# Optimization experiments

Measured on AMD Instinct MI355X. Metric: run time of the kernel, lower is better.

The kernel has to match this reference:

```python
import jax, jax.numpy as jnp
import numpy as np

B, T, H, L, FUT = 64, 256, 512, 4, 64


def setup_inputs() -> dict:
    key = jax.random.key(0)
    ks = jax.random.split(key, 8)
    s = 1.0 / np.sqrt(H)  # PyTorch LSTMCell/Linear default uniform init bound
    u = lambda k, shape: jax.random.uniform(k, shape, jnp.float32, -s, s)
    return {
        "iput": jax.random.normal(ks[0], (B, T), jnp.float32),
        "W_ih0": u(ks[1], (4 * H, 1)),        # layer 0 input->gates
        "W_ih": u(ks[2], (L - 1, 4 * H, H)),  # layers 1..L-1 input->gates
        "W_hh": u(ks[3], (L, 4 * H, H)),      # hidden->gates, all layers
        "b_ih": u(ks[4], (L, 4 * H)),
        "b_hh": u(ks[5], (L, 4 * H)),
        "W_lin": u(ks[6], (1, H)),            # readout Linear(H, 1)
        "b_lin": u(ks[7], (1,)),
        "future": FUT,
    }


def _cell(x, h, c, Wi, Wh, bi, bh):
    # PyTorch LSTMCell: gates ordered i, f, g, o
    g = x @ Wi.T + h @ Wh.T + bi + bh  # [B, 4H]
    i, f, gg, o = jnp.split(g, 4, axis=-1)
    c2 = jax.nn.sigmoid(f) * c + jax.nn.sigmoid(i) * jnp.tanh(gg)
    h2 = jax.nn.sigmoid(o) * jnp.tanh(c2)
    return h2, c2


def reference(iput, W_ih0, W_ih, W_hh, b_ih, b_hh, W_lin, b_lin, future):
    Lc = W_hh.shape[0]
    Bsz = iput.shape[0]
    Hd = W_hh.shape[-1]

    def layers(x, hs, cs):  # x: [B,1]; hs,cs: [L,B,H]
        for j in range(Lc):
            Wi = W_ih0 if j == 0 else W_ih[j - 1]
            inp = x if j == 0 else hs[j - 1]
            h2, c2 = _cell(inp, hs[j], cs[j], Wi, W_hh[j], b_ih[j], b_hh[j])
            hs = hs.at[j].set(h2)
            cs = cs.at[j].set(c2)
        return hs, cs

    hs0 = jnp.zeros((Lc, Bsz, Hd), iput.dtype)
    cs0 = jnp.zeros_like(hs0)

    def step_in(carry, x_t):  # x_t: [B]
        hs, cs = carry
        hs, cs = layers(x_t[:, None], hs, cs)
        out = hs[-1] @ W_lin.T + b_lin  # [B,1]
        return (hs, cs), out[:, 0]

    (hs, cs), outs = jax.lax.scan(step_in, (hs0, cs0), iput.T)  # outs: [T,B]

    def step_fut(carry, _):
        hs, cs, out = carry
        hs, cs = layers(out, hs, cs)
        out2 = hs[-1] @ W_lin.T + b_lin
        return (hs, cs, out2), out2[:, 0]

    last_out = outs[-1][:, None]  # feed last prediction back
    _, fouts = jax.lax.scan(step_fut, (hs, cs, last_out), None, length=future)

    return jnp.concatenate([outs, fouts], axis=0).T  # [B, T+future]
```

## Files before the change

kernel.cpp:

```cpp
#include <hip/hip_runtime.h>

#define Bsz 64
#define Tn 256
#define Hn 512
#define Ln 4
#define Gn 2048
#define TTn 320
#define NBLK 256
#define NTHR 1024
#define HB (Hn * Bsz)
#define LHB (Ln * HB)
#define NPH_W (Tn + Ln - 1)

typedef float f32x4 __attribute__((ext_vector_type(4)));

#define OFF_WHH  0
#define OFF_WIH  (OFF_WHH + Ln * 8 * Hn)
#define OFF_PART (OFF_WIH + (Ln - 1) * 8 * Hn)
#define OFF_BS   (OFF_PART + 4 * 8 * Bsz)
#define OFF_W0   (OFF_BS + Ln * 8)
#define OFF_WLIN (OFF_W0 + 8)
#define OFF_RP   (OFF_WLIN + Hn)
#define OFF_XS   (OFF_RP + 16 * Bsz)
#define OFF_C    (OFF_XS + Bsz)
#define SMEM_FLOATS (OFF_C + Ln * 2 * Bsz)
#define SMEM_BYTES (SMEM_FLOATS * 4)

#define WS_BCOUNT   0
#define WS_ARRIVE   16
#define WS_MASTER   (16 + 16 * 32)
#define WS_BOOT     (WS_MASTER + 32)
#define WS_BOOTFLAG (WS_BOOT + 32)
#define WS_U32S     (WS_BOOTFLAG + 32)

__device__ float g_h[2 * LHB];
__device__ float g_hist[Tn * HB];
__device__ float g_p[Bsz * NBLK];
__device__ float g_xsg[Bsz];

__device__ __forceinline__ float sigm(float x) { return 1.0f / (1.0f + expf(-x)); }

__device__ __forceinline__ void fma4v(f32x4& a, const f32x4 h, const float w) {
    a.x = fmaf(h.x, w, a.x); a.y = fmaf(h.y, w, a.y);
    a.z = fmaf(h.z, w, a.z); a.w = fmaf(h.w, w, a.w);
}

#define GSTF(ptr, val) \
    asm volatile("global_store_dword %0, %1, off sc0 sc1" \
                 :: "v"(ptr), "v"(val) : "memory")
#define VMWAIT() asm volatile("s_waitcnt vmcnt(0)" ::: "memory")
#define L1INV() asm volatile("buffer_inv" ::: "memory")

__device__ __forceinline__ uint32_t rmw_add(uint32_t* p, uint32_t v) {
    return __hip_atomic_fetch_add(p, v, __ATOMIC_RELAXED, __HIP_MEMORY_SCOPE_AGENT);
}
__device__ __forceinline__ uint32_t ald(const uint32_t* p) {
    return __hip_atomic_load(p, __ATOMIC_RELAXED, __HIP_MEMORY_SCOPE_AGENT);
}
__device__ __forceinline__ uint32_t xcc_id() {
    uint32_t x;
    asm("s_getreg_b32 %0, hwreg(HW_REG_XCC_ID)" : "=s"(x));
    return x & 15u;
}

__device__ __forceinline__ void boot_bar(uint32_t* wsb, int tid) {
    VMWAIT();
    __syncthreads();
    if (tid == 0) {
        __builtin_amdgcn_fence(__ATOMIC_RELEASE, "agent");
        uint32_t old = rmw_add(wsb + WS_BOOT, 1u);
        if (old == NBLK - 1u) rmw_add(wsb + WS_BOOTFLAG, 1u);
        while (ald(wsb + WS_BOOTFLAG) < 1u) __builtin_amdgcn_s_sleep(2);
        __builtin_amdgcn_fence(__ATOMIC_ACQUIRE, "agent");
    }
    __syncthreads();
    asm volatile("" ::: "memory");
}

__device__ __forceinline__ void gbar(uint32_t* wsb, int tid, uint32_t x,
                                     uint32_t cnt_x, uint32_t& e) {
    ++e;
    VMWAIT();
    __syncthreads();
    if (tid == 0) {
        const uint32_t tgt = e * (uint32_t)NBLK;
        uint32_t old = rmw_add(wsb + WS_ARRIVE + x * 32, 1u);
        if (old == e * cnt_x - 1u) {
            __builtin_amdgcn_fence(__ATOMIC_ACQUIRE, "agent");
            VMWAIT();
            rmw_add(wsb + WS_MASTER, cnt_x);
            while (ald(wsb + WS_MASTER) < tgt) {}
        } else {
            while (ald(wsb + WS_MASTER) < tgt) {}
            L1INV();
            VMWAIT();
        }
    }
    __syncthreads();
    asm volatile("" ::: "memory");
}

template <int NITER>
__device__ __forceinline__ void gemm_rows2(const float* __restrict__ wrow,
                                           const float* __restrict__ hbase,
                                           int k0, int rot, int b4,
                                           f32x4& a0, f32x4& a1) {
#pragma unroll 4
    for (int c = 0; c < NITER; ++c) {
        const int cc = (c + rot) & (NITER - 1);
        const int k = k0 + cc * 4;
        const float* hp = hbase + (size_t)k * Bsz + b4;
        const f32x4 h0 = *(const f32x4*)(hp);
        const f32x4 h1 = *(const f32x4*)(hp + Bsz);
        const f32x4 h2 = *(const f32x4*)(hp + 2 * Bsz);
        const f32x4 h3 = *(const f32x4*)(hp + 3 * Bsz);
        const f32x4 w0 = *(const f32x4*)(wrow + k);
        const f32x4 w1 = *(const f32x4*)(wrow + Hn + k);
        fma4v(a0, h0, w0.x); fma4v(a0, h1, w0.y);
        fma4v(a0, h2, w0.z); fma4v(a0, h3, w0.w);
        fma4v(a1, h0, w1.x); fma4v(a1, h1, w1.y);
        fma4v(a1, h2, w1.z); fma4v(a1, h3, w1.w);
    }
}

__device__ __forceinline__ void wave_reduce2(f32x4& a0, f32x4& a1) {
    a0.x += __shfl_xor(a0.x, 16); a0.y += __shfl_xor(a0.y, 16);
    a0.z += __shfl_xor(a0.z, 16); a0.w += __shfl_xor(a0.w, 16);
    a1.x += __shfl_xor(a1.x, 16); a1.y += __shfl_xor(a1.y, 16);
    a1.z += __shfl_xor(a1.z, 16); a1.w += __shfl_xor(a1.w, 16);
    a0.x += __shfl_xor(a0.x, 32); a0.y += __shfl_xor(a0.y, 32);
    a0.z += __shfl_xor(a0.z, 32); a0.w += __shfl_xor(a0.w, 32);
    a1.x += __shfl_xor(a1.x, 32); a1.y += __shfl_xor(a1.y, 32);
    a1.z += __shfl_xor(a1.z, 32); a1.w += __shfl_xor(a1.w, 32);
}

__global__ __launch_bounds__(NTHR, 1)
void lstm_seq(const float* __restrict__ iput,
              const float* __restrict__ Wih0,
              const float* __restrict__ Wih,
              const float* __restrict__ Whh,
              const float* __restrict__ bih,
              const float* __restrict__ bhh,
              const float* __restrict__ Wlin,
              const float* __restrict__ blin,
              float* __restrict__ out,
              uint32_t* __restrict__ wsb)
{
    extern __shared__ float sm[];
    const int bi  = blockIdx.x;
    const int tid = threadIdx.x;
    uint32_t e = 0;

    const uint32_t x = xcc_id();
    uint32_t cnt_x = 0;
    if (tid == 0) rmw_add(wsb + WS_BCOUNT + x, 1u);

    for (int i = tid; i < Ln * 8 * Hn; i += NTHR) {
        const int lyr = i >> 12, rem = i & 4095, r = rem >> 9, k = rem & 511;
        sm[OFF_WHH + i] = Whh[((size_t)(lyr * Gn + (r & 3) * Hn + bi * 2 + (r >> 2))) * Hn + k];
    }
    for (int i = tid; i < (Ln - 1) * 8 * Hn; i += NTHR) {
        const int lyr = i >> 12, rem = i & 4095, r = rem >> 9, k = rem & 511;
        sm[OFF_WIH + i] = Wih[((size_t)(lyr * Gn + (r & 3) * Hn + bi * 2 + (r >> 2))) * Hn + k];
    }
    if (tid < Ln * 8) {
        const int lyr = tid >> 3, r = tid & 7;
        const int gg = lyr * Gn + (r & 3) * Hn + bi * 2 + (r >> 2);
        sm[OFF_BS + tid] = bih[gg] + bhh[gg];
    }
    if (tid < 8) sm[OFF_W0 + tid] = Wih0[(tid & 3) * Hn + bi * 2 + (tid >> 2)];
    for (int i = tid; i < Hn; i += NTHR) sm[OFF_WLIN + i] = Wlin[i];
    for (int i = tid; i < Ln * 2 * Bsz; i += NTHR) sm[OFF_C + i] = 0.0f;

    for (int i = bi * NTHR + tid; i < 2 * LHB; i += NBLK * NTHR)
        GSTF(&g_h[i], 0.0f);

    const float blin0 = blin[0];
    boot_bar(wsb, tid);
    if (tid == 0) cnt_x = ald(wsb + WS_BCOUNT + x);

    {
        const int l   = tid >> 8;
        const int sub = tid & 255;
        const int bgw = sub & 15, b4w = bgw * 4;
        const int kq  = (sub >> 4) & 3;
        const int w2  = sub >> 6;
        const int k0w = kq * 128;
        const int r0  = w2 * 2;

        for (int s = 0; s < NPH_W; ++s) {
            const int pp = s & 1;
            float* cur        = g_h + pp * LHB;
            const float* prev = g_h + (pp ^ 1) * LHB;
            const int t = s - l;
            const bool act = ((unsigned)t < (unsigned)Tn);

            f32x4 a0 = {0.f, 0.f, 0.f, 0.f}, a1 = {0.f, 0.f, 0.f, 0.f};
            if (act) {
                gemm_rows2<32>(sm + OFF_WHH + (l * 8 + r0) * Hn,
                               prev + (size_t)l * HB, k0w, kq, b4w, a0, a1);
                if (l > 0)
                    gemm_rows2<32>(sm + OFF_WIH + ((l - 1) * 8 + r0) * Hn,
                                   prev + (size_t)(l - 1) * HB, k0w, kq, b4w, a0, a1);
            }
            wave_reduce2(a0, a1);
            if ((tid & 48) == 0) {
                *(f32x4*)&sm[OFF_PART + ((l * 8 + r0 + 0) * Bsz) + b4w] = a0;
                *(f32x4*)&sm[OFF_PART + ((l * 8 + r0 + 1) * Bsz) + b4w] = a1;
            }
            __syncthreads();

            if (tid < 512) {
                const int lb = tid >> 7, jl = (tid >> 6) & 1, b = tid & 63;
                const int tb = s - lb;
                if ((unsigned)tb < (unsigned)Tn) {
                    const int jg = bi * 2 + jl;
                    float gv[4];
#pragma unroll
                    for (int q = 0; q < 4; ++q) {
                        const int r = (jl << 2) | q;
                        gv[q] = sm[OFF_BS + lb * 8 + r]
                              + sm[OFF_PART + (lb * 8 + r) * Bsz + b];
                    }
                    if (lb == 0) {
                        const float xv = iput[b * Tn + s];
#pragma unroll
                        for (int q = 0; q < 4; ++q)
                            gv[q] = fmaf(xv, sm[OFF_W0 + ((jl << 2) | q)], gv[q]);
                    }
                    const float i_ = sigm(gv[0]);
                    const float f_ = sigm(gv[1]);
                    const float g_ = tanhf(gv[2]);
                    const float o_ = sigm(gv[3]);
                    float* cp = sm + OFF_C + (lb * 2 + jl) * Bsz + b;
                    const float c2 = fmaf(f_, *cp, i_ * g_);
                    *cp = c2;
                    const float h2 = o_ * tanhf(c2);
                    GSTF(&cur[((size_t)lb * Hn + jg) * Bsz + b], h2);
                    if (lb == 3)
                        GSTF(&g_hist[((size_t)tb * Hn + jg) * Bsz + b], h2);
                }
            }
            gbar(wsb, tid, x, cnt_x, e);
        }
    }

    {
        const int b = tid & 63, jq = tid >> 6;
        const float* hp = g_hist + ((size_t)bi * Hn + jq * 32) * Bsz + b;
        const float* wp = sm + OFF_WLIN + jq * 32;
        float r = 0.0f;
#pragma unroll 8
        for (int j = 0; j < 32; ++j) r = fmaf(hp[j * Bsz], wp[j], r);
        sm[OFF_RP + jq * Bsz + b] = r;
        if (tid < 256) {
            const int li = (tid >> 7) * 2 + 1;
            const int jl = (tid >> 6) & 1, bb = tid & 63;
            const size_t o = ((size_t)li * Hn + bi * 2 + jl) * Bsz + bb;
            const float v = g_h[o];
            GSTF(&g_h[LHB + o], v);
        }
        __syncthreads();
        if (tid < Bsz) {
            float xx = blin0;
#pragma unroll
            for (int q = 0; q < 16; ++q) xx += sm[OFF_RP + q * Bsz + tid];
            out[tid * TTn + bi] = xx;
            if (bi == 255) GSTF(&g_xsg[tid], xx);
        }
        gbar(wsb, tid, x, cnt_x, e);
    }

    {
        const int bg  = tid & 15, b4 = bg * 4;
        const int kq2 = (tid >> 4) & 3;
        const int w   = tid >> 6;
        const int r0  = (w & 3) * 2;
        const int kh  = w >> 2;
        const int k0  = kh * 128 + kq2 * 32;

        for (int t = Tn; t < TTn; ++t) {
            const int ci = t & 1;
            float* hcur        = g_h + ci * LHB;
            const float* hprev = g_h + (ci ^ 1) * LHB;

            for (int lyr = 0; lyr < Ln; ++lyr) {
                if (lyr == 0 && tid < Bsz) {
                    float xx;
                    if (t == Tn) {
                        xx = g_xsg[tid];
                    } else {
                        const f32x4* pp2 = (const f32x4*)(g_p + tid * NBLK);
                        f32x4 s4 = {0.f, 0.f, 0.f, 0.f};
#pragma unroll 16
                        for (int q = 0; q < NBLK / 4; ++q) s4 += pp2[q];
                        xx = s4.x + s4.y + s4.z + s4.w + blin0;
                        if (bi == ((t - 1) & 255))
                            out[tid * TTn + (t - 1)] = xx;
                    }
                    sm[OFF_XS + tid] = xx;
                }

                f32x4 a0 = {0.f, 0.f, 0.f, 0.f}, a1 = {0.f, 0.f, 0.f, 0.f};
                if (lyr > 0)
                    gemm_rows2<8>(sm + OFF_WIH + ((lyr - 1) * 8 + r0) * Hn,
                                  hcur + (size_t)(lyr - 1) * HB, k0, kq2, b4, a0, a1);
                gemm_rows2<8>(sm + OFF_WHH + (lyr * 8 + r0) * Hn,
                              hprev + (size_t)lyr * HB, k0, kq2, b4, a0, a1);

                wave_reduce2(a0, a1);
                if ((tid & 48) == 0) {
                    *(f32x4*)&sm[OFF_PART + ((kh * 8 + r0 + 0) * Bsz) + b4] = a0;
                    *(f32x4*)&sm[OFF_PART + ((kh * 8 + r0 + 1) * Bsz) + b4] = a1;
                }
                __syncthreads();

                float h2 = 0.0f;
                if (tid < 128) {
                    const int jl = tid >> 6, b = tid & 63;
                    const int jg = bi * 2 + jl;
                    float gv[4];
#pragma unroll
                    for (int q = 0; q < 4; ++q) {
                        const int r = (jl << 2) | q;
                        float v = sm[OFF_BS + lyr * 8 + r];
#pragma unroll
                        for (int p = 0; p < 4; ++p)
                            v += sm[OFF_PART + (p * 8 + r) * Bsz + b];
                        if (lyr == 0)
                            v = fmaf(sm[OFF_XS + b], sm[OFF_W0 + r], v);
                        gv[q] = v;
                    }
                    const float i_ = sigm(gv[0]);
                    const float f_ = sigm(gv[1]);
                    const float g_ = tanhf(gv[2]);
                    const float o_ = sigm(gv[3]);
                    float* cp = sm + OFF_C + (lyr * 2 + jl) * Bsz + b;
                    const float c2 = fmaf(f_, *cp, i_ * g_);
                    *cp = c2;
                    h2 = o_ * tanhf(c2);
                    GSTF(&hcur[((size_t)lyr * Hn + jg) * Bsz + b], h2);
                    if (lyr == 3 && jl == 1)
                        sm[OFF_RP + b] = h2 * sm[OFF_WLIN + jg];
                }
                if (lyr == 3) {
                    __syncthreads();
                    if (tid < Bsz) {
                        const float pv = fmaf(h2, sm[OFF_WLIN + bi * 2], sm[OFF_RP + tid]);
                        GSTF(&g_p[tid * NBLK + bi], pv);
                    }
                }

                gbar(wsb, tid, x, cnt_x, e);
            }
        }
    }

    if (bi == 0 && tid < Bsz) {
        const f32x4* pp2 = (const f32x4*)(g_p + tid * NBLK);
        f32x4 s4 = {0.f, 0.f, 0.f, 0.f};
#pragma unroll 16
        for (int q = 0; q < NBLK / 4; ++q) s4 += pp2[q];
        out[tid * TTn + (TTn - 1)] = s4.x + s4.y + s4.z + s4.w + blin0;
    }
}

extern "C" void kernel_launch(void* const* d_in, const int* in_sizes, int n_in,
                              void* d_out, int out_size, void* d_ws, size_t ws_size,
                              hipStream_t stream) {
    const float* iput = (const float*)d_in[0];
    const float* Wih0 = (const float*)d_in[1];
    const float* Wih  = (const float*)d_in[2];
    const float* Whh  = (const float*)d_in[3];
    const float* bih  = (const float*)d_in[4];
    const float* bhh  = (const float*)d_in[5];
    const float* Wlin = (const float*)d_in[6];
    const float* blin = (const float*)d_in[7];
    float* out = (float*)d_out;
    uint32_t* wsb = (uint32_t*)d_ws;

    (void)hipFuncSetAttribute((const void*)lstm_seq,
                              hipFuncAttributeMaxDynamicSharedMemorySize, SMEM_BYTES);

    (void)hipMemsetAsync(d_ws, 0, WS_U32S * sizeof(uint32_t), stream);

    void* args[] = {&iput, &Wih0, &Wih, &Whh, &bih, &bhh, &Wlin, &blin, &out, &wsb};
    hipLaunchCooperativeKernel((const void*)lstm_seq, dim3(NBLK), dim3(NTHR), args,
                               SMEM_BYTES, stream);
}
```

Before: 10.34 ms.

## Compute all eight gate rows per thread to reuse hidden-state loads across rows

Each thread now accumulates all 8 gate rows for its k-slice instead of 2 rows. Every loaded h vector is reused across 8 weight rows, cutting global/L2 loads of the hidden state by four. The k-dimension is split across more waves instead, so the partial-sum buffer grows to 16 slices and the gate stage sums 4 or 16 partials. This raises register pressure (32 accumulators) and adds more shuffle reductions and shared-memory stores.

```diff
diff --git a/kernel.cpp b/kernel.cpp
--- a/kernel.cpp
+++ b/kernel.cpp
@@ -17,7 +17,7 @@
 #define OFF_WHH  0
 #define OFF_WIH  (OFF_WHH + Ln * 8 * Hn)
 #define OFF_PART (OFF_WIH + (Ln - 1) * 8 * Hn)
-#define OFF_BS   (OFF_PART + 4 * 8 * Bsz)
+#define OFF_BS   (OFF_PART + 16 * 8 * Bsz)
 #define OFF_W0   (OFF_BS + Ln * 8)
 #define OFF_WLIN (OFF_W0 + 8)
 #define OFF_RP   (OFF_WLIN + Hn)
@@ -101,11 +101,10 @@
 }
 
 template <int NITER>
-__device__ __forceinline__ void gemm_rows2(const float* __restrict__ wrow,
+__device__ __forceinline__ void gemm_rows8(const float* __restrict__ w8,
                                            const float* __restrict__ hbase,
-                                           int k0, int rot, int b4,
-                                           f32x4& a0, f32x4& a1) {
-#pragma unroll 4
+                                           int k0, int rot, int b4, f32x4* acc) {
+#pragma unroll
     for (int c = 0; c < NITER; ++c) {
         const int cc = (c + rot) & (NITER - 1);
         const int k = k0 + cc * 4;
@@ -114,24 +113,25 @@
         const f32x4 h1 = *(const f32x4*)(hp + Bsz);
         const f32x4 h2 = *(const f32x4*)(hp + 2 * Bsz);
         const f32x4 h3 = *(const f32x4*)(hp + 3 * Bsz);
-        const f32x4 w0 = *(const f32x4*)(wrow + k);
-        const f32x4 w1 = *(const f32x4*)(wrow + Hn + k);
-        fma4v(a0, h0, w0.x); fma4v(a0, h1, w0.y);
-        fma4v(a0, h2, w0.z); fma4v(a0, h3, w0.w);
-        fma4v(a1, h0, w1.x); fma4v(a1, h1, w1.y);
-        fma4v(a1, h2, w1.z); fma4v(a1, h3, w1.w);
-    }
-}
-
-__device__ __forceinline__ void wave_reduce2(f32x4& a0, f32x4& a1) {
-    a0.x += __shfl_xor(a0.x, 16); a0.y += __shfl_xor(a0.y, 16);
-    a0.z += __shfl_xor(a0.z, 16); a0.w += __shfl_xor(a0.w, 16);
-    a1.x += __shfl_xor(a1.x, 16); a1.y += __shfl_xor(a1.y, 16);
-    a1.z += __shfl_xor(a1.z, 16); a1.w += __shfl_xor(a1.w, 16);
-    a0.x += __shfl_xor(a0.x, 32); a0.y += __shfl_xor(a0.y, 32);
-    a0.z += __shfl_xor(a0.z, 32); a0.w += __shfl_xor(a0.w, 32);
-    a1.x += __shfl_xor(a1.x, 32); a1.y += __shfl_xor(a1.y, 32);
-    a1.z += __shfl_xor(a1.z, 32); a1.w += __shfl_xor(a1.w, 32);
+#pragma unroll
+        for (int r = 0; r < 8; ++r) {
+            const f32x4 wv = *(const f32x4*)(w8 + r * Hn + k);
+            fma4v(acc[r], h0, wv.x); fma4v(acc[r], h1, wv.y);
+            fma4v(acc[r], h2, wv.z); fma4v(acc[r], h3, wv.w);
+        }
+    }
+}
+
+__device__ __forceinline__ void wave_reduce8(f32x4* acc) {
+#pragma unroll
+    for (int r = 0; r < 8; ++r) {
+        f32x4 a = acc[r];
+        a.x += __shfl_xor(a.x, 16); a.y += __shfl_xor(a.y, 16);
+        a.z += __shfl_xor(a.z, 16); a.w += __shfl_xor(a.w, 16);
+        a.x += __shfl_xor(a.x, 32); a.y += __shfl_xor(a.y, 32);
+        a.z += __shfl_xor(a.z, 32); a.w += __shfl_xor(a.w, 32);
+        acc[r] = a;
+    }
 }
 
 __global__ __launch_bounds__(NTHR, 1)
@@ -180,13 +180,13 @@
     if (tid == 0) cnt_x = ald(wsb + WS_BCOUNT + x);
 
     {
-        const int l   = tid >> 8;
-        const int sub = tid & 255;
-        const int bgw = sub & 15, b4w = bgw * 4;
-        const int kq  = (sub >> 4) & 3;
-        const int w2  = sub >> 6;
-        const int k0w = kq * 128;
-        const int r0  = w2 * 2;
+        const int w   = tid >> 6;
+        const int l   = w >> 2;
+        const int kq  = w & 3;
+        const int bgw = tid & 15, b4w = bgw * 4;
+        const int ks  = (tid >> 4) & 3;
+        const int k0w = kq * 128 + ks * 32;
+        const int rot = ks * 2;
 
         for (int s = 0; s < NPH_W; ++s) {
             const int pp = s & 1;
@@ -195,18 +195,22 @@
             const int t = s - l;
             const bool act = ((unsigned)t < (unsigned)Tn);
 
-            f32x4 a0 = {0.f, 0.f, 0.f, 0.f}, a1 = {0.f, 0.f, 0.f, 0.f};
+            f32x4 acc[8];
+#pragma unroll
+            for (int r = 0; r < 8; ++r) acc[r] = (f32x4){0.f, 0.f, 0.f, 0.f};
+
             if (act) {
-                gemm_rows2<32>(sm + OFF_WHH + (l * 8 + r0) * Hn,
-                               prev + (size_t)l * HB, k0w, kq, b4w, a0, a1);
+                gemm_rows8<8>(sm + OFF_WHH + l * 8 * Hn,
+                              prev + (size_t)l * HB, k0w, rot, b4w, acc);
                 if (l > 0)
-                    gemm_rows2<32>(sm + OFF_WIH + ((l - 1) * 8 + r0) * Hn,
-                                   prev + (size_t)(l - 1) * HB, k0w, kq, b4w, a0, a1);
+                    gemm_rows8<8>(sm + OFF_WIH + (l - 1) * 8 * Hn,
+                                  prev + (size_t)(l - 1) * HB, k0w, rot, b4w, acc);
             }
-            wave_reduce2(a0, a1);
+            wave_reduce8(acc);
             if ((tid & 48) == 0) {
-                *(f32x4*)&sm[OFF_PART + ((l * 8 + r0 + 0) * Bsz) + b4w] = a0;
-                *(f32x4*)&sm[OFF_PART + ((l * 8 + r0 + 1) * Bsz) + b4w] = a1;
+#pragma unroll
+                for (int r = 0; r < 8; ++r)
+                    *(f32x4*)&sm[OFF_PART + ((w * 8 + r) * Bsz) + b4w] = acc[r];
             }
             __syncthreads();
 
@@ -219,8 +223,11 @@
 #pragma unroll
                     for (int q = 0; q < 4; ++q) {
                         const int r = (jl << 2) | q;
-                        gv[q] = sm[OFF_BS + lb * 8 + r]
-                              + sm[OFF_PART + (lb * 8 + r) * Bsz + b];
+                        float v = sm[OFF_BS + lb * 8 + r];
+#pragma unroll
+                        for (int p = 0; p < 4; ++p)
+                            v += sm[OFF_PART + (((lb * 4 + p) * 8 + r) * Bsz) + b];
+                        gv[q] = v;
                     }
                     if (lb == 0) {
                         const float xv = iput[b * Tn + s];
@@ -273,11 +280,10 @@
 
     {
         const int bg  = tid & 15, b4 = bg * 4;
-        const int kq2 = (tid >> 4) & 3;
+        const int ks  = (tid >> 4) & 3;
         const int w   = tid >> 6;
-        const int r0  = (w & 3) * 2;
-        const int kh  = w >> 2;
-        const int k0  = kh * 128 + kq2 * 32;
+        const int k0  = w * 32 + ks * 8;
+        const int rot = ks & 1;
 
         for (int t = Tn; t < TTn; ++t) {
             const int ci = t & 1;
@@ -301,17 +307,21 @@
                     sm[OFF_XS + tid] = xx;
                 }
 
-                f32x4 a0 = {0.f, 0.f, 0.f, 0.f}, a1 = {0.f, 0.f, 0.f, 0.f};
+                f32x4 acc[8];
+#pragma unroll
+                for (int r = 0; r < 8; ++r) acc[r] = (f32x4){0.f, 0.f, 0.f, 0.f};
+
                 if (lyr > 0)
-                    gemm_rows2<8>(sm + OFF_WIH + ((lyr - 1) * 8 + r0) * Hn,
-                                  hcur + (size_t)(lyr - 1) * HB, k0, kq2, b4, a0, a1);
-                gemm_rows2<8>(sm + OFF_WHH + (lyr * 8 + r0) * Hn,
-                              hprev + (size_t)lyr * HB, k0, kq2, b4, a0, a1);
-
-                wave_reduce2(a0, a1);
+                    gemm_rows8<2>(sm + OFF_WIH + (lyr - 1) * 8 * Hn,
+                                  hcur + (size_t)(lyr - 1) * HB, k0, rot, b4, acc);
+                gemm_rows8<2>(sm + OFF_WHH + lyr * 8 * Hn,
+                              hprev + (size_t)lyr * HB, k0, rot, b4, acc);
+
+                wave_reduce8(acc);
                 if ((tid & 48) == 0) {
-                    *(f32x4*)&sm[OFF_PART + ((kh * 8 + r0 + 0) * Bsz) + b4] = a0;
-                    *(f32x4*)&sm[OFF_PART + ((kh * 8 + r0 + 1) * Bsz) + b4] = a1;
+#pragma unroll
+                    for (int r = 0; r < 8; ++r)
+                        *(f32x4*)&sm[OFF_PART + ((w * 8 + r) * Bsz) + b4] = acc[r];
                 }
                 __syncthreads();
 
@@ -325,8 +335,8 @@
                         const int r = (jl << 2) | q;
                         float v = sm[OFF_BS + lyr * 8 + r];
 #pragma unroll
-                        for (int p = 0; p < 4; ++p)
-                            v += sm[OFF_PART + (p * 8 + r) * Bsz + b];
+                        for (int p = 0; p < 16; ++p)
+                            v += sm[OFF_PART + ((p * 8 + r) * Bsz) + b];
                         if (lyr == 0)
                             v = fmaf(sm[OFF_XS + b], sm[OFF_W0 + r], v);
                         gv[q] = v;
```

New measurement: 14.09 ms. 36.3% more time.
